# Performance work log

Hardware: AMD Instinct MI355X
Metric: run time of the kernel (lower is better)

## Reference

```python
import jax, jax.numpy as jnp
import numpy as np

N_NODES = 50000
N_EDGES = 1600000
IN_CH = 128
HID = 32
HEADS = 3
OUT_CH = 32
NEG_SLOPE = 0.2


def setup_inputs() -> dict:
    key = jax.random.key(0)
    ks = jax.random.split(key, 12)
    s = 0.05
    x = jax.random.normal(ks[0], (N_NODES, IN_CH), dtype=jnp.float32)
    edge_index = jax.random.randint(ks[1], (2, N_EDGES), 0, N_NODES, dtype=jnp.int64)
    W1 = jax.random.normal(ks[2], (IN_CH, HEADS * HID), dtype=jnp.float32) * s
    att_src1 = jax.random.normal(ks[3], (HEADS, HID), dtype=jnp.float32) * s
    att_dst1 = jax.random.normal(ks[4], (HEADS, HID), dtype=jnp.float32) * s
    b1 = jnp.zeros((HEADS * HID,), dtype=jnp.float32)
    W2 = jax.random.normal(ks[5], (HEADS * HID, OUT_CH), dtype=jnp.float32) * s
    att_src2 = jax.random.normal(ks[6], (1, OUT_CH), dtype=jnp.float32) * s
    att_dst2 = jax.random.normal(ks[7], (1, OUT_CH), dtype=jnp.float32) * s
    b2 = jnp.zeros((OUT_CH,), dtype=jnp.float32)
    Wp = jax.random.normal(ks[8], (OUT_CH, 1), dtype=jnp.float32) * s
    bp = jnp.zeros((1,), dtype=jnp.float32)
    return dict(x=x, edge_index=edge_index, W1=W1, att_src1=att_src1,
                att_dst1=att_dst1, b1=b1, W2=W2, att_src2=att_src2,
                att_dst2=att_dst2, b2=b2, Wp=Wp, bp=bp)


def gat_layer(x, src, dst, W, a_src, a_dst, b, heads, out_ch, concat):
    # PyG GATConv semantics: per-head linear, edge attention with leaky_relu,
    # softmax over incoming edges per destination node, scatter-add aggregate.
    N = x.shape[0]
    h = (x @ W).reshape(N, heads, out_ch)                 # [N,H,C]
    a_s = jnp.einsum('nhc,hc->nh', h, a_src)              # [N,H]
    a_d = jnp.einsum('nhc,hc->nh', h, a_dst)              # [N,H]
    e = jax.nn.leaky_relu(a_s[src] + a_d[dst], NEG_SLOPE) # [E,H]
    m = jax.ops.segment_max(e, dst, num_segments=N)       # stable softmax per dst
    p = jnp.exp(e - m[dst])
    s = jax.ops.segment_sum(p, dst, num_segments=N)
    alpha = p / (s[dst] + 1e-16)                          # [E,H]
    msg = h[src] * alpha[:, :, None]                      # [E,H,C]
    out = jax.ops.segment_sum(msg, dst, num_segments=N)   # [N,H,C]
    out = out.reshape(N, heads * out_ch) if concat else out.mean(axis=1)
    return out + b


def reference(x, edge_index, W1, att_src1, att_dst1, b1, W2, att_src2,
              att_dst2, b2, Wp, bp):
    N = x.shape[0]
    loop = jnp.arange(N, dtype=edge_index.dtype)
    src = jnp.concatenate([edge_index[0], loop])  # add self-loops (PyG default)
    dst = jnp.concatenate([edge_index[1], loop])
    h = gat_layer(x, src, dst, W1, att_src1, att_dst1, b1, HEADS, HID, True)
    h = jax.nn.elu(h)
    h = gat_layer(h, src, dst, W2, att_src2, att_dst2, b2, 1, OUT_CH, False)
    prob = jax.nn.sigmoid(h @ Wp + bp)                    # [N,1]
    return prob
```

## Files before the change

### kernel.cpp

```cpp
#include <hip/hip_runtime.h>
#include <hip/hip_bf16.h>
#include <math.h>


#define IN_CH 128
#define HID 32
#define HEADS 3
#define OUT_CH 32
#define NEG_SLOPE 0.2f

#define NBUCK_SHIFT 6
#define NBUCK_NODES 64
#define BCAP 2560
#define EPB 4096

typedef unsigned int uint;
typedef unsigned short ushort;
typedef short v8s __attribute__((ext_vector_type(8)));
typedef float v4f __attribute__((ext_vector_type(4)));

static __device__ __forceinline__ uint f2bf(float f) {
    uint u = __float_as_uint(f);
    return (u + 0x7FFFu + ((u >> 16) & 1u)) >> 16;
}
static __device__ __forceinline__ uint pk4fp8(float a, float b, float c, float d) {
    int r = 0;
    r = __builtin_amdgcn_cvt_pk_fp8_f32(a, b, r, false);
    r = __builtin_amdgcn_cvt_pk_fp8_f32(c, d, r, true);
    return (uint)r;
}
static __device__ __forceinline__ float elu_f(float o) {
    return o > 0.f ? o : __expf(o) - 1.f;
}
static __device__ __forceinline__ float frcp(float x) {
    return __builtin_amdgcn_rcpf(x);
}

#define LDA 136
#define LDC 100


__global__ __launch_bounds__(256) void k_g1b(const float* __restrict__ x,
                                             const float* __restrict__ W1,
                                             const float* __restrict__ as,
                                             const float* __restrict__ ad,
                                             uint* __restrict__ h1u,
                                             float* __restrict__ a_d1p,
                                             const int* __restrict__ ei,
                                             int E, int Etot, int B2, int G1,
                                             int* __restrict__ gcur,
                                             uint* __restrict__ stage, int N) {
    __shared__ __attribute__((aligned(16))) char raw[(64 * LDA + 96 * LDA) * 2];
    int tid = threadIdx.x;

    if ((int)blockIdx.x >= G1) {
        int* hist     = (int*)raw;
        int* runStart = hist + 1024;
        int* rankCtr  = runStart + 1024;
        for (int i = tid; i < 1024; i += 256) { hist[i] = 0; rankCtr[i] = 0; }
        __syncthreads();
        int base = ((int)blockIdx.x - G1) * EPB;

        uint rec[16];
        #pragma unroll
        for (int i = 0; i < 16; ++i) {
            int e = base + tid + i * 256;
            uint r = 0xFFFFFFFFu;
            if (e < Etot) {
                int s, d;
                if (e < E) { s = ei[e]; d = ei[E + e]; }
                else       { s = e - E; d = s; }
                r = ((uint)d << 16) | (uint)s;
                atomicAdd(&hist[d >> NBUCK_SHIFT], 1);
            }
            rec[i] = r;
        }
        __syncthreads();
        for (int i = tid; i < B2; i += 256) {
            int c = hist[i];
            if (c) runStart[i] = atomicAdd(&gcur[i], c);
        }
        __syncthreads();
        #pragma unroll
        for (int i = 0; i < 16; ++i) {
            uint r = rec[i];
            if (r != 0xFFFFFFFFu) {
                int b = (int)(r >> 16) >> NBUCK_SHIFT;
                int pos = runStart[b] + atomicAdd(&rankCtr[b], 1);
                if (pos < BCAP)
                    stage[(size_t)b * BCAP + pos] = r & 0x003FFFFFu;
            }
        }
        return;
    }

    ushort* sA  = (ushort*)raw;
    ushort* sBT = sA + 64 * LDA;
    float*  sC  = (float*)raw;
    int b0 = blockIdx.x * 64;

    uint* sA32 = (uint*)sA;
    #pragma unroll
    for (int i = 0; i < 8; ++i) {
        int g = tid + i * 256;
        int row = g >> 5, c4 = g & 31;
        float4 v = make_float4(0.f, 0.f, 0.f, 0.f);
        int gn = b0 + row;
        if (gn < N) v = *(const float4*)(x + (size_t)gn * IN_CH + c4 * 4);
        sA32[row * 68 + c4 * 2]     = f2bf(v.x) | (f2bf(v.y) << 16);
        sA32[row * 68 + c4 * 2 + 1] = f2bf(v.z) | (f2bf(v.w) << 16);
    }
    #pragma unroll
    for (int i = 0; i < 12; ++i) {
        int g = tid + i * 256;
        int k = g / 24, c4 = (g - k * 24) * 4;
        float4 v = *(const float4*)(W1 + k * 96 + c4);
        sBT[(c4 + 0) * LDA + k] = (ushort)f2bf(v.x);
        sBT[(c4 + 1) * LDA + k] = (ushort)f2bf(v.y);
        sBT[(c4 + 2) * LDA + k] = (ushort)f2bf(v.z);
        sBT[(c4 + 3) * LDA + k] = (ushort)f2bf(v.w);
    }
    __syncthreads();

    int l = tid & 63, w = tid >> 6;
    int m15 = l & 15, q = l >> 4;

    v8s afr[4];
    const ushort* arow = sA + (w * 16 + m15) * LDA + q * 8;
    #pragma unroll
    for (int kc = 0; kc < 4; ++kc) afr[kc] = *(const v8s*)(arow + kc * 32);

    v4f acc[6];
    #pragma unroll
    for (int cg = 0; cg < 6; ++cg) {
        acc[cg] = (v4f){0.f, 0.f, 0.f, 0.f};
        const ushort* brow = sBT + (cg * 16 + m15) * LDA + q * 8;
        #pragma unroll
        for (int kc = 0; kc < 4; ++kc) {
            v8s bfr = *(const v8s*)(brow + kc * 32);
            acc[cg] = __builtin_amdgcn_mfma_f32_16x16x32_bf16(afr[kc], bfr, acc[cg], 0, 0, 0);
        }
    }
    __syncthreads();
    #pragma unroll
    for (int cg = 0; cg < 6; ++cg) {
        int col = cg * 16 + m15;
        #pragma unroll
        for (int r = 0; r < 4; ++r)
            sC[(w * 16 + q * 4 + r) * LDC + col] = acc[cg][r];
    }
    __syncthreads();

    if (tid < 192) {
        int ln = tid / 3, h = tid - ln * 3;
        int node = b0 + ln;
        if (node < N) {
            const float* vs = as + h * 32;
            const float* vd = ad + h * 32;
            const float* row = sC + ln * LDC + h * 32;
            float s = 0.f, d = 0.f;
            #pragma unroll
            for (int c = 0; c < 32; ++c) { float v = row[c]; s += v * vs[c]; d += v * vd[c]; }
            ((float*)h1u)[(size_t)node * 32 + 24 + h] = s;
            a_d1p[node * 4 + h] = d;
        }
    }
    {
        int node = tid >> 2, part = tid & 3;
        int gn = b0 + node;
        if (gn < N) {
            const float* row = sC + node * LDC + part * 24;
            uint tmp[6];
            #pragma unroll
            for (int j = 0; j < 6; ++j)
                tmp[j] = pk4fp8(row[4*j], row[4*j+1], row[4*j+2], row[4*j+3]);
            uint* dst = h1u + (size_t)gn * 32 + part * 6;
            *(uint2*)(dst + 0) = make_uint2(tmp[0], tmp[1]);
            *(uint2*)(dst + 2) = make_uint2(tmp[2], tmp[3]);
            *(uint2*)(dst + 4) = make_uint2(tmp[4], tmp[5]);
        }
    }
}


__global__ __launch_bounds__(256) void k_sort(const uint* __restrict__ stage,
                                              const int* __restrict__ gcur,
                                              int* __restrict__ offs,
                                              uint* __restrict__ edges,
                                              int N, int Etot, int B2) {
    __shared__ uint items[BCAP];
    __shared__ int red[256];
    __shared__ int lofs[NBUCK_NODES + 1];
    __shared__ int cursors[NBUCK_NODES];
    int t = threadIdx.x;
    int b = blockIdx.x;

    int partial = 0;
    for (int i = t; i < b; i += 256) partial += gcur[i];
    red[t] = partial;
    if (t < NBUCK_NODES) cursors[t] = 0;
    __syncthreads();
    #pragma unroll
    for (int s = 128; s > 0; s >>= 1) {
        if (t < s) red[t] += red[t + s];
        __syncthreads();
    }
    int gbase = red[0];
    int cnt = gcur[b]; if (cnt > BCAP) cnt = BCAP;

    for (int i = t; i < cnt; i += 256) items[i] = stage[(size_t)b * BCAP + i];
    __syncthreads();
    for (int i = t; i < cnt; i += 256) atomicAdd(&cursors[items[i] >> 16], 1);
    __syncthreads();
    if (t == 0) {
        int run = 0;
        for (int i = 0; i < NBUCK_NODES; ++i) { int v = cursors[i]; lofs[i] = run; run += v; }
        lofs[NBUCK_NODES] = run;
    }
    __syncthreads();
    int nodeBase = b << NBUCK_SHIFT;
    if (t < NBUCK_NODES && nodeBase + t < N) offs[nodeBase + t] = gbase + lofs[t];
    if (b == B2 - 1 && t == 0) offs[N] = Etot;
    if (t < NBUCK_NODES) cursors[t] = 0;
    __syncthreads();
    uint addHi = (uint)nodeBase << 16;
    for (int i = t; i < cnt; i += 256) {
        uint it = items[i];
        int ln = (int)(it >> 16);
        int r = atomicAdd(&cursors[ln], 1);
        edges[gbase + lofs[ln] + r] = it + addHi;
    }
}


#define W2LD 36

#define A1_BODY(EIDX)                                                          \
    {                                                                          \
        uint pk = edges[EIDX];                                                 \
        uint src = pk & 0xFFFFu;                                               \
        const uint* hr = h1u + src * 32u;                                      \
        const float4 af = *(const float4*)(hr + 24);                           \
        float z0 = af.x + adv.x, z1 = af.y + adv.y, z2 = af.z + adv.z;         \
        z0 = fmaxf(z0, NEG_SLOPE * z0);                                        \
        z1 = fmaxf(z1, NEG_SLOPE * z1);                                        \
        z2 = fmaxf(z2, NEG_SLOPE * z2);                                        \
        float p0 = __expf(z0), p1 = __expf(z1), p2 = __expf(z2);               \
        uint w0 = hr[d], w1 = hr[d + 8], w2 = hr[d + 16];                      \
        { auto lo = __builtin_amdgcn_cvt_pk_f32_fp8((int)w0, false);           \
          auto hi = __builtin_amdgcn_cvt_pk_f32_fp8((int)w0, true);            \
          a00 += p0 * lo[0]; a01 += p0 * lo[1];                                \
          a02 += p0 * hi[0]; a03 += p0 * hi[1]; }                              \
        { auto lo = __builtin_amdgcn_cvt_pk_f32_fp8((int)w1, false);           \
          auto hi = __builtin_amdgcn_cvt_pk_f32_fp8((int)w1, true);            \
          a10 += p1 * lo[0]; a11 += p1 * lo[1];                                \
          a12 += p1 * hi[0]; a13 += p1 * hi[1]; }                              \
        { auto lo = __builtin_amdgcn_cvt_pk_f32_fp8((int)w2, false);           \
          auto hi = __builtin_amdgcn_cvt_pk_f32_fp8((int)w2, true);            \
          a20 += p2 * lo[0]; a21 += p2 * lo[1];                                \
          a22 += p2 * hi[0]; a23 += p2 * hi[1]; }                              \
        d0 += p0; d1 += p1; d2 += p2;                                          \
    }

__global__ __launch_bounds__(256) void k_agg1g2(const int* __restrict__ offs,
                                                const uint* __restrict__ edges,
                                                const uint* __restrict__ h1u,
                                                const float* __restrict__ a_d1p,
                                                const float* __restrict__ b1,
                                                const float* __restrict__ W2,
                                                const float* __restrict__ as2,
                                                const float* __restrict__ ad2,
                                                uint* __restrict__ h2u,
                                                float* __restrict__ a_d2, int N) {
    __shared__ __attribute__((aligned(16))) float sW2[96 * W2LD];
    __shared__ float ss2[32], sd2[32];
    __shared__ float rowbuf[4][96];

    int tid = threadIdx.x;
    #pragma unroll
    for (int i = 0; i < 3; ++i) {
        int g = tid + i * 256;
        int k = g >> 3, c4i = g & 7;
        *(float4*)&sW2[k * W2LD + c4i * 4] = *(const float4*)(W2 + k * 32 + c4i * 4);
    }
    if (tid < 32) { ss2[tid] = as2[tid]; sd2[tid] = ad2[tid]; }
    __syncthreads();

    int w = tid >> 6;
    int node = blockIdx.x * 4 + w;
    if (node >= N) return;
    int lane = tid & 63;
    int g = lane >> 3, d = lane & 7;
    const float4 adv = *(const float4*)(a_d1p + node * 4);

    int off0 = offs[node], off1 = offs[node + 1];
    int deg = off1 - off0;
    int fullEnd = off0 + (deg & ~7);
    float a00 = 0.f, a01 = 0.f, a02 = 0.f, a03 = 0.f;
    float a10 = 0.f, a11 = 0.f, a12 = 0.f, a13 = 0.f;
    float a20 = 0.f, a21 = 0.f, a22 = 0.f, a23 = 0.f;
    float d0 = 0.f, d1 = 0.f, d2 = 0.f;

    #pragma unroll 2
    for (int e0 = off0; e0 < fullEnd; e0 += 8) A1_BODY((uint)(e0 + g))
    if (g < (deg & 7)) A1_BODY((uint)(fullEnd + g))

    #define REDF(v) { v += __shfl_xor(v, 8); v += __shfl_xor(v, 16); v += __shfl_xor(v, 32); }
    REDF(a00) REDF(a01) REDF(a02) REDF(a03)
    REDF(a10) REDF(a11) REDF(a12) REDF(a13)
    REDF(a20) REDF(a21) REDF(a22) REDF(a23)
    REDF(d0) REDF(d1) REDF(d2)
    #undef REDF

    if (lane < 8) {
        float r0 = frcp(d0 + 1e-16f);
        float r1 = frcp(d1 + 1e-16f);
        float r2 = frcp(d2 + 1e-16f);
        float4 bv0 = *(const float4*)(b1 + 4 * lane);
        float4 bv1 = *(const float4*)(b1 + 32 + 4 * lane);
        float4 bv2 = *(const float4*)(b1 + 64 + 4 * lane);
        float4 v;
        v.x = elu_f(a00 * r0 + bv0.x);
        v.y = elu_f(a01 * r0 + bv0.y);
        v.z = elu_f(a02 * r0 + bv0.z);
        v.w = elu_f(a03 * r0 + bv0.w);
        *(float4*)&rowbuf[w][4 * lane] = v;
        v.x = elu_f(a10 * r1 + bv1.x);
        v.y = elu_f(a11 * r1 + bv1.y);
        v.z = elu_f(a12 * r1 + bv1.z);
        v.w = elu_f(a13 * r1 + bv1.w);
        *(float4*)&rowbuf[w][32 + 4 * lane] = v;
        v.x = elu_f(a20 * r2 + bv2.x);
        v.y = elu_f(a21 * r2 + bv2.y);
        v.z = elu_f(a22 * r2 + bv2.z);
        v.w = elu_f(a23 * r2 + bv2.w);
        *(float4*)&rowbuf[w][64 + 4 * lane] = v;
    }

    int c4 = lane & 7, kg = lane >> 3;
    float4 accv = make_float4(0.f, 0.f, 0.f, 0.f);
    const float* rb = &rowbuf[w][kg * 12];
    const float* wb = &sW2[kg * 12 * W2LD + c4 * 4];
    #pragma unroll 12
    for (int i = 0; i < 12; ++i) {
        float rv = rb[i];
        float4 wv = *(const float4*)(wb + i * W2LD);
        accv.x += rv * wv.x; accv.y += rv * wv.y;
        accv.z += rv * wv.z; accv.w += rv * wv.w;
    }
    #define REDF(c) { c += __shfl_xor(c, 8); c += __shfl_xor(c, 16); c += __shfl_xor(c, 32); }
    REDF(accv.x) REDF(accv.y) REDF(accv.z) REDF(accv.w)
    #undef REDF

    float4 sv = *(const float4*)&ss2[c4 * 4];
    float4 dv = *(const float4*)&sd2[c4 * 4];
    float ps = accv.x * sv.x + accv.y * sv.y + accv.z * sv.z + accv.w * sv.w;
    float pd = accv.x * dv.x + accv.y * dv.y + accv.z * dv.z + accv.w * dv.w;
    ps += __shfl_xor(ps, 1); ps += __shfl_xor(ps, 2); ps += __shfl_xor(ps, 4);
    pd += __shfl_xor(pd, 1); pd += __shfl_xor(pd, 2); pd += __shfl_xor(pd, 4);
    if (lane < 8) {
        h2u[(size_t)node * 16 + c4] = pk4fp8(accv.x, accv.y, accv.z, accv.w);
        if (lane == 0) {
            ((float*)h2u)[(size_t)node * 16 + 8] = ps;
            a_d2[node] = pd;
        }
    }
}


#define A2_BODY(EIDX)                                                          \
    {                                                                          \
        uint pk = edges[EIDX];                                                 \
        uint src = pk & 0xFFFFu;                                               \
        const uint* hr = h2u + src * 16u;                                      \
        float z = *(const float*)(hr + 8) + ad2u;                              \
        z = fmaxf(z, NEG_SLOPE * z);                                           \
        float p = __expf(z);                                                   \
        uint wv = hr[d];                                                       \
        auto lo = __builtin_amdgcn_cvt_pk_f32_fp8((int)wv, false);             \
        auto hi = __builtin_amdgcn_cvt_pk_f32_fp8((int)wv, true);              \
        c0 += p * lo[0]; c1 += p * lo[1];                                      \
        c2 += p * hi[0]; c3 += p * hi[1];                                      \
        den += p;                                                              \
    }

__global__ __launch_bounds__(256) void k_agg2f(const int* __restrict__ offs,
                                               const uint* __restrict__ edges,
                                               const uint* __restrict__ h2u,
                                               const float* __restrict__ a_d2,
                                               const float* __restrict__ b2,
                                               const float* __restrict__ Wp,
                                               const float* __restrict__ bp,
                                               float* __restrict__ out, int N) {
    int node = blockIdx.x * 4 + (threadIdx.x >> 6);
    if (node >= N) return;
    int lane = threadIdx.x & 63;
    int g = lane >> 3, d = lane & 7;
    const float ad2u = a_d2[node];

    int off0 = offs[node], off1 = offs[node + 1];
    int deg = off1 - off0;
    int fullEnd = off0 + (deg & ~7);
    float c0 = 0.f, c1 = 0.f, c2 = 0.f, c3 = 0.f, den = 0.f;

    #pragma unroll 2
    for (int e0 = off0; e0 < fullEnd; e0 += 8) A2_BODY((uint)(e0 + g))
    if (g < (deg & 7)) A2_BODY((uint)(fullEnd + g))

    #define REDF(v) { v += __shfl_xor(v, 8); v += __shfl_xor(v, 16); v += __shfl_xor(v, 32); }
    REDF(c0) REDF(c1) REDF(c2) REDF(c3) REDF(den)
    #undef REDF

    float4 bv = *(const float4*)(b2 + 4 * d);
    float4 wv = *(const float4*)(Wp + 4 * d);
    float r = frcp(den + 1e-16f);
    float v = (c0 * r + bv.x) * wv.x + (c1 * r + bv.y) * wv.y +
              (c2 * r + bv.z) * wv.z + (c3 * r + bv.w) * wv.w;
    v += __shfl_xor(v, 1);
    v += __shfl_xor(v, 2);
    v += __shfl_xor(v, 4);
    if (lane == 0)
        out[node] = frcp(1.f + __expf(-(v + bp[0])));
}


extern "C" void kernel_launch(void* const* d_in, const int* in_sizes, int n_in,
                              void* d_out, int out_size, void* d_ws, size_t ws_size,
                              hipStream_t stream) {
    const float* x      = (const float*)d_in[0];
    const int*   ei     = (const int*)d_in[1];
    const float* W1     = (const float*)d_in[2];
    const float* att_s1 = (const float*)d_in[3];
    const float* att_d1 = (const float*)d_in[4];
    const float* b1     = (const float*)d_in[5];
    const float* W2     = (const float*)d_in[6];
    const float* att_s2 = (const float*)d_in[7];
    const float* att_d2 = (const float*)d_in[8];
    const float* b2     = (const float*)d_in[9];
    const float* Wp     = (const float*)d_in[10];
    const float* bp     = (const float*)d_in[11];
    float* out = (float*)d_out;

    const int N = in_sizes[0] / IN_CH;
    const int E = in_sizes[1] / 2;
    const int Etot = E + N;
    const int B2 = (N + NBUCK_NODES - 1) >> NBUCK_SHIFT;
    const int G1 = (N + 63) / 64;
    const int BK = (Etot + EPB - 1) / EPB;

    float* ws    = (float*)d_ws;
    uint*  h1u   = (uint*)ws;
    float* a_d1p = ws + (size_t)N * 32;
    int*   offs  = (int*)(a_d1p + (size_t)N * 4);
    uint*  edges = (uint*)(offs + (N + 1));
    int*   gcur  = (int*)(edges + Etot);
    uint*  stage = (uint*)(gcur + 1024);
    uint*  h2u   = stage + (size_t)B2 * BCAP;
    float* a_d2  = (float*)(h2u + (size_t)N * 16);

    (void)hipMemsetAsync(gcur, 0, 1024 * sizeof(int), stream);

    k_g1b<<<G1 + BK, 256, 0, stream>>>(x, W1, att_s1, att_d1, h1u, a_d1p,
                                       ei, E, Etot, B2, G1, gcur, stage, N);
    k_sort<<<B2, 256, 0, stream>>>(stage, gcur, offs, edges, N, Etot, B2);

    k_agg1g2<<<(N + 3) / 4, 256, 0, stream>>>(offs, edges, h1u, a_d1p, b1, W2,
                                              att_s2, att_d2, h2u, a_d2, N);
    k_agg2f<<<(N + 3) / 4, 256, 0, stream>>>(offs, edges, h2u, a_d2,
                                             b2, Wp, bp, out, N);
}
```

Measured before the change: 226.4 us.

## Map two nodes per wavefront and shrink sorted edge indices to 16 bits

The two aggregation kernels now give each node half a wavefront (32 lanes, 4 edge groups) instead of a full wavefront. Eight nodes are processed per block, with lane predication for ragged degrees. The sorted edge list stores only the 16-bit source id, halving index traffic. The layer-1 fp8 feature layout is interleaved so each lane fetches its three head words with one 12-byte load. With average degree around 33, each half-wave runs more iterations serially, and the two halves diverge when neighbour degrees differ. The 16-bit ids only hold while the node count stays below 65536.

```diff
diff --git a/kernel.cpp b/kernel.cpp
--- a/kernel.cpp
+++ b/kernel.cpp
@@ -18,6 +18,7 @@
 typedef unsigned short ushort;
 typedef short v8s __attribute__((ext_vector_type(8)));
 typedef float v4f __attribute__((ext_vector_type(4)));
+typedef uint v3u __attribute__((ext_vector_type(3)));
 
 static __device__ __forceinline__ uint f2bf(float f) {
     uint u = __float_as_uint(f);
@@ -169,11 +170,15 @@
         int node = tid >> 2, part = tid & 3;
         int gn = b0 + node;
         if (gn < N) {
-            const float* row = sC + node * LDC + part * 24;
+            const float* row = sC + node * LDC;
             uint tmp[6];
             #pragma unroll
-            for (int j = 0; j < 6; ++j)
-                tmp[j] = pk4fp8(row[4*j], row[4*j+1], row[4*j+2], row[4*j+3]);
+            for (int jj = 0; jj < 6; ++jj) {
+                int j = part * 6 + jj;
+                int dd = j / 3, slot = j - dd * 3;
+                const float* p = row + slot * 32 + dd * 4;
+                tmp[jj] = pk4fp8(p[0], p[1], p[2], p[3]);
+            }
             uint* dst = h1u + (size_t)gn * 32 + part * 6;
             *(uint2*)(dst + 0) = make_uint2(tmp[0], tmp[1]);
             *(uint2*)(dst + 2) = make_uint2(tmp[2], tmp[3]);
@@ -186,7 +191,7 @@
 __global__ __launch_bounds__(256) void k_sort(const uint* __restrict__ stage,
                                               const int* __restrict__ gcur,
                                               int* __restrict__ offs,
-                                              uint* __restrict__ edges,
+                                              ushort* __restrict__ edges,
                                               int N, int Etot, int B2) {
     __shared__ uint items[BCAP];
     __shared__ int red[256];
@@ -223,47 +228,19 @@
     if (b == B2 - 1 && t == 0) offs[N] = Etot;
     if (t < NBUCK_NODES) cursors[t] = 0;
     __syncthreads();
-    uint addHi = (uint)nodeBase << 16;
     for (int i = t; i < cnt; i += 256) {
         uint it = items[i];
         int ln = (int)(it >> 16);
         int r = atomicAdd(&cursors[ln], 1);
-        edges[gbase + lofs[ln] + r] = it + addHi;
+        edges[gbase + lofs[ln] + r] = (ushort)(it & 0xFFFFu);
     }
 }
 
 
 #define W2LD 36
 
-#define A1_BODY(EIDX)                                                          \
-    {                                                                          \
-        uint pk = edges[EIDX];                                                 \
-        uint src = pk & 0xFFFFu;                                               \
-        const uint* hr = h1u + src * 32u;                                      \
-        const float4 af = *(const float4*)(hr + 24);                           \
-        float z0 = af.x + adv.x, z1 = af.y + adv.y, z2 = af.z + adv.z;         \
-        z0 = fmaxf(z0, NEG_SLOPE * z0);                                        \
-        z1 = fmaxf(z1, NEG_SLOPE * z1);                                        \
-        z2 = fmaxf(z2, NEG_SLOPE * z2);                                        \
-        float p0 = __expf(z0), p1 = __expf(z1), p2 = __expf(z2);               \
-        uint w0 = hr[d], w1 = hr[d + 8], w2 = hr[d + 16];                      \
-        { auto lo = __builtin_amdgcn_cvt_pk_f32_fp8((int)w0, false);           \
-          auto hi = __builtin_amdgcn_cvt_pk_f32_fp8((int)w0, true);            \
-          a00 += p0 * lo[0]; a01 += p0 * lo[1];                                \
-          a02 += p0 * hi[0]; a03 += p0 * hi[1]; }                              \
-        { auto lo = __builtin_amdgcn_cvt_pk_f32_fp8((int)w1, false);           \
-          auto hi = __builtin_amdgcn_cvt_pk_f32_fp8((int)w1, true);            \
-          a10 += p1 * lo[0]; a11 += p1 * lo[1];                                \
-          a12 += p1 * hi[0]; a13 += p1 * hi[1]; }                              \
-        { auto lo = __builtin_amdgcn_cvt_pk_f32_fp8((int)w2, false);           \
-          auto hi = __builtin_amdgcn_cvt_pk_f32_fp8((int)w2, true);            \
-          a20 += p2 * lo[0]; a21 += p2 * lo[1];                                \
-          a22 += p2 * hi[0]; a23 += p2 * hi[1]; }                              \
-        d0 += p0; d1 += p1; d2 += p2;                                          \
-    }
-
 __global__ __launch_bounds__(256) void k_agg1g2(const int* __restrict__ offs,
-                                                const uint* __restrict__ edges,
+                                                const ushort* __restrict__ edges,
                                                 const uint* __restrict__ h1u,
                                                 const float* __restrict__ a_d1p,
                                                 const float* __restrict__ b1,
@@ -274,81 +251,116 @@
                                                 float* __restrict__ a_d2, int N) {
     __shared__ __attribute__((aligned(16))) float sW2[96 * W2LD];
     __shared__ float ss2[32], sd2[32];
-    __shared__ float rowbuf[4][96];
+    __shared__ float rowbuf[8][96];
 
     int tid = threadIdx.x;
     #pragma unroll
     for (int i = 0; i < 3; ++i) {
-        int g = tid + i * 256;
-        int k = g >> 3, c4i = g & 7;
+        int gg = tid + i * 256;
+        int k = gg >> 3, c4i = gg & 7;
         *(float4*)&sW2[k * W2LD + c4i * 4] = *(const float4*)(W2 + k * 32 + c4i * 4);
     }
     if (tid < 32) { ss2[tid] = as2[tid]; sd2[tid] = ad2[tid]; }
     __syncthreads();
 
     int w = tid >> 6;
-    int node = blockIdx.x * 4 + w;
-    if (node >= N) return;
     int lane = tid & 63;
-    int g = lane >> 3, d = lane & 7;
-    const float4 adv = *(const float4*)(a_d1p + node * 4);
-
-    int off0 = offs[node], off1 = offs[node + 1];
+    int half = lane >> 5, hl = lane & 31;
+    int node = blockIdx.x * 8 + w * 2 + half;
+    bool nvalid = node < N;
+    int nodeC = nvalid ? node : (N - 1);
+    int g = hl >> 3, d = hl & 7;
+    const float4 adv = *(const float4*)(a_d1p + nodeC * 4);
+
+    int off0 = offs[nodeC], off1 = offs[nodeC + 1];
     int deg = off1 - off0;
-    int fullEnd = off0 + (deg & ~7);
+    if (deg < 0) deg = 0;
+    int nIt = (deg + 3) >> 2;
+    int nItO = __shfl_xor(nIt, 32);
+    int itMax = nIt > nItO ? nIt : nItO;
+
     float a00 = 0.f, a01 = 0.f, a02 = 0.f, a03 = 0.f;
     float a10 = 0.f, a11 = 0.f, a12 = 0.f, a13 = 0.f;
     float a20 = 0.f, a21 = 0.f, a22 = 0.f, a23 = 0.f;
     float d0 = 0.f, d1 = 0.f, d2 = 0.f;
 
     #pragma unroll 2
-    for (int e0 = off0; e0 < fullEnd; e0 += 8) A1_BODY((uint)(e0 + g))
-    if (g < (deg & 7)) A1_BODY((uint)(fullEnd + g))
-
-    #define REDF(v) { v += __shfl_xor(v, 8); v += __shfl_xor(v, 16); v += __shfl_xor(v, 32); }
+    for (int i = 0; i < itMax; ++i) {
+        int e = i * 4 + g;
+        bool act = e < deg;
+        int eidx = off0 + (act ? e : 0);
+        uint src = (uint)edges[eidx];
+        const uint* hr = h1u + src * 32u;
+        float4 af = *(const float4*)(hr + 24);
+        v3u wv = *(const v3u*)(hr + 3 * d);
+        float z0 = af.x + adv.x, z1 = af.y + adv.y, z2 = af.z + adv.z;
+        z0 = fmaxf(z0, NEG_SLOPE * z0);
+        z1 = fmaxf(z1, NEG_SLOPE * z1);
+        z2 = fmaxf(z2, NEG_SLOPE * z2);
+        float p0 = __expf(z0), p1 = __expf(z1), p2 = __expf(z2);
+        p0 = act ? p0 : 0.f;
+        p1 = act ? p1 : 0.f;
+        p2 = act ? p2 : 0.f;
+        { auto lo = __builtin_amdgcn_cvt_pk_f32_fp8((int)wv[0], false);
+          auto hi = __builtin_amdgcn_cvt_pk_f32_fp8((int)wv[0], true);
+          a00 += p0 * lo[0]; a01 += p0 * lo[1];
+          a02 += p0 * hi[0]; a03 += p0 * hi[1]; }
+        { auto lo = __builtin_amdgcn_cvt_pk_f32_fp8((int)wv[1], false);
+          auto hi = __builtin_amdgcn_cvt_pk_f32_fp8((int)wv[1], true);
+          a10 += p1 * lo[0]; a11 += p1 * lo[1];
+          a12 += p1 * hi[0]; a13 += p1 * hi[1]; }
+        { auto lo = __builtin_amdgcn_cvt_pk_f32_fp8((int)wv[2], false);
+          auto hi = __builtin_amdgcn_cvt_pk_f32_fp8((int)wv[2], true);
+          a20 += p2 * lo[0]; a21 += p2 * lo[1];
+          a22 += p2 * hi[0]; a23 += p2 * hi[1]; }
+        d0 += p0; d1 += p1; d2 += p2;
+    }
+
+    #define REDF(v) { v += __shfl_xor(v, 8); v += __shfl_xor(v, 16); }
     REDF(a00) REDF(a01) REDF(a02) REDF(a03)
     REDF(a10) REDF(a11) REDF(a12) REDF(a13)
     REDF(a20) REDF(a21) REDF(a22) REDF(a23)
     REDF(d0) REDF(d1) REDF(d2)
     #undef REDF
 
-    if (lane < 8) {
+    int rbrow = w * 2 + half;
+    if (hl < 8) {
         float r0 = frcp(d0 + 1e-16f);
         float r1 = frcp(d1 + 1e-16f);
         float r2 = frcp(d2 + 1e-16f);
-        float4 bv0 = *(const float4*)(b1 + 4 * lane);
-        float4 bv1 = *(const float4*)(b1 + 32 + 4 * lane);
-        float4 bv2 = *(const float4*)(b1 + 64 + 4 * lane);
+        float4 bv0 = *(const float4*)(b1 + 4 * hl);
+        float4 bv1 = *(const float4*)(b1 + 32 + 4 * hl);
+        float4 bv2 = *(const float4*)(b1 + 64 + 4 * hl);
         float4 v;
         v.x = elu_f(a00 * r0 + bv0.x);
         v.y = elu_f(a01 * r0 + bv0.y);
         v.z = elu_f(a02 * r0 + bv0.z);
         v.w = elu_f(a03 * r0 + bv0.w);
-        *(float4*)&rowbuf[w][4 * lane] = v;
+        *(float4*)&rowbuf[rbrow][4 * hl] = v;
         v.x = elu_f(a10 * r1 + bv1.x);
         v.y = elu_f(a11 * r1 + bv1.y);
         v.z = elu_f(a12 * r1 + bv1.z);
         v.w = elu_f(a13 * r1 + bv1.w);
-        *(float4*)&rowbuf[w][32 + 4 * lane] = v;
+        *(float4*)&rowbuf[rbrow][32 + 4 * hl] = v;
         v.x = elu_f(a20 * r2 + bv2.x);
         v.y = elu_f(a21 * r2 + bv2.y);
         v.z = elu_f(a22 * r2 + bv2.z);
         v.w = elu_f(a23 * r2 + bv2.w);
-        *(float4*)&rowbuf[w][64 + 4 * lane] = v;
-    }
-
-    int c4 = lane & 7, kg = lane >> 3;
+        *(float4*)&rowbuf[rbrow][64 + 4 * hl] = v;
+    }
+
+    int c4 = hl & 7, kg = hl >> 3;
     float4 accv = make_float4(0.f, 0.f, 0.f, 0.f);
-    const float* rb = &rowbuf[w][kg * 12];
-    const float* wb = &sW2[kg * 12 * W2LD + c4 * 4];
-    #pragma unroll 12
-    for (int i = 0; i < 12; ++i) {
+    const float* rb = &rowbuf[rbrow][kg * 24];
+    const float* wb = &sW2[kg * 24 * W2LD + c4 * 4];
+    #pragma unroll 24
+    for (int i = 0; i < 24; ++i) {
         float rv = rb[i];
-        float4 wv = *(const float4*)(wb + i * W2LD);
-        accv.x += rv * wv.x; accv.y += rv * wv.y;
-        accv.z += rv * wv.z; accv.w += rv * wv.w;
-    }
-    #define REDF(c) { c += __shfl_xor(c, 8); c += __shfl_xor(c, 16); c += __shfl_xor(c, 32); }
+        float4 wvv = *(const float4*)(wb + i * W2LD);
+        accv.x += rv * wvv.x; accv.y += rv * wvv.y;
+        accv.z += rv * wvv.z; accv.w += rv * wvv.w;
+    }
+    #define REDF(c) { c += __shfl_xor(c, 8); c += __shfl_xor(c, 16); }
     REDF(accv.x) REDF(accv.y) REDF(accv.z) REDF(accv.w)
     #undef REDF
 
@@ -358,9 +370,9 @@
     float pd = accv.x * dv.x + accv.y * dv.y + accv.z * dv.z + accv.w * dv.w;
     ps += __shfl_xor(ps, 1); ps += __shfl_xor(ps, 2); ps += __shfl_xor(ps, 4);
     pd += __shfl_xor(pd, 1); pd += __shfl_xor(pd, 2); pd += __shfl_xor(pd, 4);
-    if (lane < 8) {
+    if (nvalid && hl < 8) {
         h2u[(size_t)node * 16 + c4] = pk4fp8(accv.x, accv.y, accv.z, accv.w);
-        if (lane == 0) {
+        if (hl == 0) {
             ((float*)h2u)[(size_t)node * 16 + 8] = ps;
             a_d2[node] = pd;
         }
@@ -368,46 +380,54 @@
 }
 
 
-#define A2_BODY(EIDX)                                                          \
-    {                                                                          \
-        uint pk = edges[EIDX];                                                 \
-        uint src = pk & 0xFFFFu;                                               \
-        const uint* hr = h2u + src * 16u;                                      \
-        float z = *(const float*)(hr + 8) + ad2u;                              \
-        z = fmaxf(z, NEG_SLOPE * z);                                           \
-        float p = __expf(z);                                                   \
-        uint wv = hr[d];                                                       \
-        auto lo = __builtin_amdgcn_cvt_pk_f32_fp8((int)wv, false);             \
-        auto hi = __builtin_amdgcn_cvt_pk_f32_fp8((int)wv, true);              \
-        c0 += p * lo[0]; c1 += p * lo[1];                                      \
-        c2 += p * hi[0]; c3 += p * hi[1];                                      \
-        den += p;                                                              \
-    }
-
 __global__ __launch_bounds__(256) void k_agg2f(const int* __restrict__ offs,
-                                               const uint* __restrict__ edges,
+                                               const ushort* __restrict__ edges,
                                                const uint* __restrict__ h2u,
                                                const float* __restrict__ a_d2,
                                                const float* __restrict__ b2,
                                                const float* __restrict__ Wp,
                                                const float* __restrict__ bp,
                                                float* __restrict__ out, int N) {
-    int node = blockIdx.x * 4 + (threadIdx.x >> 6);
-    if (node >= N) return;
-    int lane = threadIdx.x & 63;
-    int g = lane >> 3, d = lane & 7;
-    const float ad2u = a_d2[node];
-
-    int off0 = offs[node], off1 = offs[node + 1];
+    int tid = threadIdx.x;
+    int w = tid >> 6;
+    int lane = tid & 63;
+    int half = lane >> 5, hl = lane & 31;
+    int node = blockIdx.x * 8 + w * 2 + half;
+    bool nvalid = node < N;
+    int nodeC = nvalid ? node : (N - 1);
+    int g = hl >> 3, d = hl & 7;
+    const float ad2u = a_d2[nodeC];
+
+    int off0 = offs[nodeC], off1 = offs[nodeC + 1];
     int deg = off1 - off0;
-    int fullEnd = off0 + (deg & ~7);
+    if (deg < 0) deg = 0;
+    int nIt = (deg + 3) >> 2;
+    int nItO = __shfl_xor(nIt, 32);
+    int itMax = nIt > nItO ? nIt : nItO;
+
     float c0 = 0.f, c1 = 0.f, c2 = 0.f, c3 = 0.f, den = 0.f;
 
     #pragma unroll 2
-    for (int e0 = off0; e0 < fullEnd; e0 += 8) A2_BODY((uint)(e0 + g))
-    if (g < (deg & 7)) A2_BODY((uint)(fullEnd + g))
-
-    #define REDF(v) { v += __shfl_xor(v, 8); v += __shfl_xor(v, 16); v += __shfl_xor(v, 32); }
+    for (int i = 0; i < itMax; ++i) {
+        int e = i * 4 + g;
+        bool act = e < deg;
+        int eidx = off0 + (act ? e : 0);
+        uint src = (uint)edges[eidx];
+        const uint* hr = h2u + src * 16u;
+        float zf = *(const float*)(hr + 8);
+        uint wvv = hr[d];
+        float z = zf + ad2u;
+        z = fmaxf(z, NEG_SLOPE * z);
+        float p = __expf(z);
+        p = act ? p : 0.f;
+        auto lo = __builtin_amdgcn_cvt_pk_f32_fp8((int)wvv, false);
+        auto hi = __builtin_amdgcn_cvt_pk_f32_fp8((int)wvv, true);
+        c0 += p * lo[0]; c1 += p * lo[1];
+        c2 += p * hi[0]; c3 += p * hi[1];
+        den += p;
+    }
+
+    #define REDF(v) { v += __shfl_xor(v, 8); v += __shfl_xor(v, 16); }
     REDF(c0) REDF(c1) REDF(c2) REDF(c3) REDF(den)
     #undef REDF
 
@@ -419,7 +439,7 @@
     v += __shfl_xor(v, 1);
     v += __shfl_xor(v, 2);
     v += __shfl_xor(v, 4);
-    if (lane == 0)
+    if (nvalid && hl == 0)
         out[node] = frcp(1.f + __expf(-(v + bp[0])));
 }
 
@@ -448,15 +468,15 @@
     const int G1 = (N + 63) / 64;
     const int BK = (Etot + EPB - 1) / EPB;
 
-    float* ws    = (float*)d_ws;
-    uint*  h1u   = (uint*)ws;
-    float* a_d1p = ws + (size_t)N * 32;
-    int*   offs  = (int*)(a_d1p + (size_t)N * 4);
-    uint*  edges = (uint*)(offs + (N + 1));
-    int*   gcur  = (int*)(edges + Etot);
-    uint*  stage = (uint*)(gcur + 1024);
-    uint*  h2u   = stage + (size_t)B2 * BCAP;
-    float* a_d2  = (float*)(h2u + (size_t)N * 16);
+    float*  ws    = (float*)d_ws;
+    uint*   h1u   = (uint*)ws;
+    float*  a_d1p = ws + (size_t)N * 32;
+    int*    offs  = (int*)(a_d1p + (size_t)N * 4);
+    ushort* edges = (ushort*)(offs + (N + 1));
+    int*    gcur  = (int*)(edges + (((size_t)Etot + 1) & ~(size_t)1));
+    uint*   stage = (uint*)(gcur + 1024);
+    uint*   h2u   = stage + (size_t)B2 * BCAP;
+    float*  a_d2  = (float*)(h2u + (size_t)N * 16);
 
     (void)hipMemsetAsync(gcur, 0, 1024 * sizeof(int), stream);
 
@@ -464,8 +484,8 @@
                                        ei, E, Etot, B2, G1, gcur, stage, N);
     k_sort<<<B2, 256, 0, stream>>>(stage, gcur, offs, edges, N, Etot, B2);
 
-    k_agg1g2<<<(N + 3) / 4, 256, 0, stream>>>(offs, edges, h1u, a_d1p, b1, W2,
+    k_agg1g2<<<(N + 7) / 8, 256, 0, stream>>>(offs, edges, h1u, a_d1p, b1, W2,
                                               att_s2, att_d2, h2u, a_d2, N);
-    k_agg2f<<<(N + 3) / 4, 256, 0, stream>>>(offs, edges, h2u, a_d2,
+    k_agg2f<<<(N + 7) / 8, 256, 0, stream>>>(offs, edges, h2u, a_d2,
                                              b2, Wp, bp, out, N);
 }
```

Result: faster. 201.7 us (-10.9%).
